# Kernel tuning notes

Hardware: AMD Instinct MI355X
Metric: run time of the kernel (lower is better)

## Reference

```python
import jax, jax.numpy as jnp
import numpy as np

PATCH = 12
IN_CH = 1
EMBED = 96
K_NEIGH = 5
N_NODES = 1024
B = 4
L_TIME = 2016  # 12 * 168 patches
CIN = IN_CH * (K_NEIGH + 1)


def setup_inputs() -> dict:
    key = jax.random.key(0)
    k1, k2, k3, k4 = jax.random.split(key, 4)
    long_term_history = jax.random.normal(k1, (B, N_NODES, IN_CH, L_TIME), dtype=jnp.float32)
    # positive adjacency weights (used as multinomial sampling probabilities)
    adj_mx = jax.random.uniform(k2, (N_NODES, N_NODES), dtype=jnp.float32, minval=1e-3, maxval=1.0)
    # Conv2d(in=CIN, out=EMBED, kernel=(PATCH,1)) -> weight [EMBED, CIN, PATCH]
    conv_w = jax.random.normal(k3, (EMBED, CIN, PATCH), dtype=jnp.float32) * 0.02
    conv_b = jax.random.normal(k4, (EMBED,), dtype=jnp.float32) * 0.02
    return {"long_term_history": long_term_history, "adj_mx": adj_mx,
            "conv_w": conv_w, "conv_b": conv_b}


def _sample_k_neighbors(adj_mx, k, key):
    # per-row multinomial with replacement via the Gumbel-max trick
    logits = jnp.log(adj_mx)                      # row-normalization is a constant shift
    g = jax.random.gumbel(key, (adj_mx.shape[0], k, adj_mx.shape[1]), dtype=adj_mx.dtype)
    return jnp.argmax(logits[:, None, :] + g, axis=-1)  # [N, k] int


def reference(long_term_history, adj_mx, conv_w, conv_b):
    b, n, c, lt = long_term_history.shape
    # adj_adjust_u = 1, adj_adjust_v = 0 (adjust_adj_mx=False) -> adjusted adj == adj
    sampled = _sample_k_neighbors(adj_mx, K_NEIGH, jax.random.key(42))  # [N, K]
    # batched neighbor gather: [B, N, K, C, L] -> [B, N, K*C, L]
    nb = long_term_history[:, sampled].reshape(b, n, K_NEIGH * c, lt)
    data = jnp.concatenate([long_term_history, nb], axis=2)  # [B, N, (K+1)*C, L]
    # patchify conv: kernel (PATCH,1), stride (PATCH,1) == per-patch GEMM
    p = lt // PATCH
    patches = data.reshape(b, n, CIN, p, PATCH)              # [B,N,Cin,P,patch]
    out = jnp.einsum('bncpt,oct->bnop', patches, conv_w) + conv_b[None, None, :, None]
    return out  # [B, N, EMBED, P]
```

## Files before the change

kernel.cpp:

```cpp
#include <hip/hip_runtime.h>
#include <cstdint>
#include <cstddef>

#define N_NODES 1024
#define K_NEIGH 5
#define L_TIME  2016
#define PATCHSZ 12
#define EMBED   96
#define CINX    6
#define P_CNT   168
#define KDOT    72
#define OUT_PER_BN (EMBED * P_CNT)

#define WS_WH 24576
#define WS_WL (24576 + 18432)

typedef __attribute__((ext_vector_type(8))) short   bf16x8;
typedef __attribute__((ext_vector_type(4))) float   f32x4;
typedef __attribute__((ext_vector_type(4))) unsigned int u32x4;

__device__ __forceinline__ uint32_t f2bf_bits(float f) {
  uint32_t u = __float_as_uint(f);
  return (u + 0x7fffu + ((u >> 16) & 1u)) >> 16;
}
__device__ __forceinline__ float bf_hi_f(uint32_t hb) { return __uint_as_float(hb << 16); }

__device__ __forceinline__ uint32_t rotl32(uint32_t x, int r) {
  return (x << r) | (x >> (32 - r));
}
__device__ __forceinline__ uint32_t threefry_bits(uint32_t hi, uint32_t lo) {
  const uint32_t ks0 = 0u, ks1 = 42u;
  const uint32_t ks2 = ks0 ^ ks1 ^ 0x1BD11BDAu;
  uint32_t x0 = hi + ks0, x1 = lo + ks1;
#define TF_ROUND(r) { x0 += x1; x1 = rotl32(x1, (r)); x1 ^= x0; }
  TF_ROUND(13) TF_ROUND(15) TF_ROUND(26) TF_ROUND(6)
  x0 += ks1; x1 += ks2 + 1u;
  TF_ROUND(17) TF_ROUND(29) TF_ROUND(16) TF_ROUND(24)
  x0 += ks2; x1 += ks0 + 2u;
  TF_ROUND(13) TF_ROUND(15) TF_ROUND(26) TF_ROUND(6)
  x0 += ks0; x1 += ks1 + 3u;
  TF_ROUND(17) TF_ROUND(29) TF_ROUND(16) TF_ROUND(24)
  x0 += ks1; x1 += ks2 + 4u;
  TF_ROUND(13) TF_ROUND(15) TF_ROUND(26) TF_ROUND(6)
  x0 += ks2; x1 += ks0 + 5u;
#undef TF_ROUND
  return x0 ^ x1;
}
__device__ __forceinline__ float gumbel_from_bits(uint32_t bits) {
  float f = __uint_as_float((bits >> 9) | 0x3f800000u) - 1.0f;
  f = fmaxf(f, 1.17549435e-38f);
  return -logf(-logf(f));
}

__global__ __launch_bounds__(256)
void wpack_kernel(const float* __restrict__ wgt, char* __restrict__ ws) {
  const int tid = threadIdx.x;
  for (int t = tid; t < 1152; t += 256) {
    const int L  = t & 63;
    const int mk = t >> 6;
    const int kc = mk % 3;
    const int m  = mk / 3;
    const int o  = m * 16 + (L & 15);
    const int kbase = kc * 32 + (L >> 4) * 8;
    uint32_t hb[8], lb[8];
    #pragma unroll
    for (int j = 0; j < 8; ++j) {
      const int k = kbase + j;
      float v = (k < KDOT) ? wgt[o * KDOT + k] : 0.0f;
      hb[j] = f2bf_bits(v);
      lb[j] = f2bf_bits(v - bf_hi_f(hb[j]));
    }
    u32x4 ph, pl;
    #pragma unroll
    for (int i = 0; i < 4; ++i) {
      ph[i] = hb[2*i] | (hb[2*i+1] << 16);
      pl[i] = lb[2*i] | (lb[2*i+1] << 16);
    }
    *reinterpret_cast<u32x4*>(ws + WS_WH + mk * 1024 + L * 16) = ph;
    *reinterpret_cast<u32x4*>(ws + WS_WL + mk * 1024 + L * 16) = pl;
  }
}

__global__ __launch_bounds__(1024)
void sample_kernel(const float* __restrict__ adj, int* __restrict__ sampled) {
  const int n = blockIdx.x;
  const int tid = threadIdx.x;
  const float la = logf(adj[(size_t)n * N_NODES + tid]);

  float best[K_NEIGH];
  int   bestj[K_NEIGH];
  #pragma unroll
  for (int k = 0; k < K_NEIGH; ++k) {
    uint32_t bits = threefry_bits(0u, (uint32_t)((n * K_NEIGH + k) * N_NODES + tid));
    best[k] = la + gumbel_from_bits(bits);
    bestj[k] = tid;
  }
  #pragma unroll
  for (int k = 0; k < K_NEIGH; ++k) {
    #pragma unroll
    for (int off = 32; off > 0; off >>= 1) {
      float ov = __shfl_down(best[k], off);
      int   oj = __shfl_down(bestj[k], off);
      if (ov > best[k] || (ov == best[k] && oj < bestj[k])) { best[k] = ov; bestj[k] = oj; }
    }
  }
  __shared__ float sv[16][K_NEIGH];
  __shared__ int   sj[16][K_NEIGH];
  if ((tid & 63) == 0) {
    #pragma unroll
    for (int k = 0; k < K_NEIGH; ++k) { sv[tid >> 6][k] = best[k]; sj[tid >> 6][k] = bestj[k]; }
  }
  __syncthreads();
  if (tid < K_NEIGH) {
    float b = sv[0][tid];
    int  bj = sj[0][tid];
    #pragma unroll
    for (int w = 1; w < 16; ++w) {
      if (sv[w][tid] > b || (sv[w][tid] == b && sj[w][tid] < bj)) { b = sv[w][tid]; bj = sj[w][tid]; }
    }
    sampled[n * K_NEIGH + tid] = bj;
  }
}

__global__ __launch_bounds__(256)
void embed_kernel(const float* __restrict__ hist, const char* __restrict__ ws,
                  const float* __restrict__ bias, const int* __restrict__ sampled,
                  float* __restrict__ out) {
  __shared__ __align__(16) char xlds[36864];
  char* XH = xlds;
  char* XL = xlds + 18432;

  const int tid  = threadIdx.x;
  const int L    = tid & 63;
  const int wave = tid >> 6;

  bf16x8 wh[18], wl[18];
  #pragma unroll
  for (int mk = 0; mk < 18; ++mk) {
    wh[mk] = __builtin_bit_cast(bf16x8, *reinterpret_cast<const u32x4*>(ws + WS_WH + mk*1024 + L*16));
    wl[mk] = __builtin_bit_cast(bf16x8, *reinterpret_cast<const u32x4*>(ws + WS_WL + mk*1024 + L*16));
  }
  float bv[6][4];
  #pragma unroll
  for (int m = 0; m < 6; ++m)
    #pragma unroll
    for (int i = 0; i < 4; ++i)
      bv[m][i] = bias[m * 16 + (L >> 4) * 4 + i];

  for (int bn = blockIdx.x; bn < 4 * N_NODES; bn += 512) {
    const int n = bn & (N_NODES - 1);
    const int b = bn >> 10;
    const float* rows[CINX];
    rows[0] = hist + (size_t)bn * L_TIME;
    #pragma unroll
    for (int k = 0; k < K_NEIGH; ++k)
      rows[k + 1] = hist + ((size_t)b * N_NODES + sampled[n * K_NEIGH + k]) * L_TIME;
    float* outbn = out + (size_t)bn * OUT_PER_BN;

    for (int h = 0; h < 2; ++h) {
      const int ncols  = h ? 80 : 96;
      const int ntasks = ncols * 12;
      for (int t = tid; t < ntasks; t += 256) {
        const int q   = t / ncols;
        const int ci  = t - q * ncols;
        const int p   = h * 96 + ci;
        const int ntl = ci >> 4;
        const int c16 = ci & 15;
        const int kc  = q >> 2;
        const int qg  = q & 3;
        char* dsth = XH + (ntl*3 + kc)*1024 + c16*64 + qg*16;
        char* dstl = XL + (ntl*3 + kc)*1024 + c16*64 + qg*16;
        u32x4 ph = {0,0,0,0}, pl = {0,0,0,0};
        if (q < 9 && p < P_CNT) {
          const int gk = q * 8;
          const int c0 = gk / 12,       t0 = gk - c0 * 12;
          const int c1 = (gk + 4) / 12, t1 = (gk + 4) - c1 * 12;
          const float4 f0 = *reinterpret_cast<const float4*>(rows[c0] + p * PATCHSZ + t0);
          const float4 f1 = *reinterpret_cast<const float4*>(rows[c1] + p * PATCHSZ + t1);
          const float v[8] = {f0.x, f0.y, f0.z, f0.w, f1.x, f1.y, f1.z, f1.w};
          uint32_t hb[8], lb[8];
          #pragma unroll
          for (int j = 0; j < 8; ++j) {
            hb[j] = f2bf_bits(v[j]);
            lb[j] = f2bf_bits(v[j] - bf_hi_f(hb[j]));
          }
          #pragma unroll
          for (int i = 0; i < 4; ++i) {
            ph[i] = hb[2*i] | (hb[2*i+1] << 16);
            pl[i] = lb[2*i] | (lb[2*i+1] << 16);
          }
        }
        *reinterpret_cast<u32x4*>(dsth) = ph;
        *reinterpret_cast<u32x4*>(dstl) = pl;
      }
      __syncthreads();
      const int T = h ? 5 : 6;
      for (int ntl = wave; ntl < T; ntl += 4) {
        f32x4 acc[6];
        #pragma unroll
        for (int m = 0; m < 6; ++m) acc[m] = {0.f, 0.f, 0.f, 0.f};
        #pragma unroll
        for (int kc = 0; kc < 3; ++kc) {
          const char* sh = XH + (ntl*3 + kc)*1024 + (L & 15)*64 + (L >> 4)*16;
          const char* sl = XL + (ntl*3 + kc)*1024 + (L & 15)*64 + (L >> 4)*16;
          const bf16x8 xh = __builtin_bit_cast(bf16x8, *reinterpret_cast<const u32x4*>(sh));
          const bf16x8 xl = __builtin_bit_cast(bf16x8, *reinterpret_cast<const u32x4*>(sl));
          #pragma unroll
          for (int m = 0; m < 6; ++m) {
            acc[m] = __builtin_amdgcn_mfma_f32_16x16x32_bf16(wh[m*3+kc], xh, acc[m], 0, 0, 0);
            acc[m] = __builtin_amdgcn_mfma_f32_16x16x32_bf16(wh[m*3+kc], xl, acc[m], 0, 0, 0);
            acc[m] = __builtin_amdgcn_mfma_f32_16x16x32_bf16(wl[m*3+kc], xh, acc[m], 0, 0, 0);
          }
        }
        const int p = h * 96 + ntl * 16 + (L & 15);
        if (p < P_CNT) {
          #pragma unroll
          for (int m = 0; m < 6; ++m) {
            const int o = m * 16 + (L >> 4) * 4;
            #pragma unroll
            for (int i = 0; i < 4; ++i)
              outbn[(size_t)(o + i) * P_CNT + p] = acc[m][i] + bv[m][i];
          }
        }
      }
      __syncthreads();
    }
  }
}

extern "C" void kernel_launch(void* const* d_in, const int* in_sizes, int n_in,
                              void* d_out, int out_size, void* d_ws, size_t ws_size,
                              hipStream_t stream) {
  const float* hist = (const float*)d_in[0];
  const float* adj  = (const float*)d_in[1];
  const float* wgt  = (const float*)d_in[2];
  const float* bias = (const float*)d_in[3];
  float* out = (float*)d_out;
  char* ws   = (char*)d_ws;
  int* sampled = (int*)d_ws;

  wpack_kernel<<<dim3(1), dim3(256), 0, stream>>>(wgt, ws);
  sample_kernel<<<dim3(N_NODES), dim3(1024), 0, stream>>>(adj, sampled);
  embed_kernel<<<dim3(512), dim3(256), 0, stream>>>(hist, ws, bias, sampled, out);
}
```

Measured before the change: 421.9 us.

## Load patch operands straight into MFMA registers, dropping LDS staging and barriers

Each wave now loads the input patch fragments it needs directly from global memory into registers, splits them into bf16 hi/lo, and feeds the MFMAs. This removes the shared-memory staging buffers and the two block barriers per half. The bias is folded into the accumulator's initial value, and output stores are nontemporal. The trade is a less coalesced global access pattern and no sharing of loaded data across waves, in exchange for higher occupancy and no synchronisation.

```diff
diff --git a/kernel.cpp b/kernel.cpp
--- a/kernel.cpp
+++ b/kernel.cpp
@@ -122,17 +122,28 @@
   }
 }
 
+__device__ __forceinline__ const float* sel_row(const float* r0, const float* r1,
+                                                const float* r2, const float* r3,
+                                                const float* r4, const float* r5,
+                                                int c) {
+  const float* p = r0;
+  p = (c == 1) ? r1 : p;
+  p = (c == 2) ? r2 : p;
+  p = (c == 3) ? r3 : p;
+  p = (c == 4) ? r4 : p;
+  p = (c == 5) ? r5 : p;
+  return p;
+}
+
 __global__ __launch_bounds__(256)
 void embed_kernel(const float* __restrict__ hist, const char* __restrict__ ws,
                   const float* __restrict__ bias, const int* __restrict__ sampled,
                   float* __restrict__ out) {
-  __shared__ __align__(16) char xlds[36864];
-  char* XH = xlds;
-  char* XL = xlds + 18432;
-
   const int tid  = threadIdx.x;
   const int L    = tid & 63;
   const int wave = tid >> 6;
+  const int g    = L >> 4;
+  const int col  = L & 15;
 
   bf16x8 wh[18], wl[18];
   #pragma unroll
@@ -140,43 +151,50 @@
     wh[mk] = __builtin_bit_cast(bf16x8, *reinterpret_cast<const u32x4*>(ws + WS_WH + mk*1024 + L*16));
     wl[mk] = __builtin_bit_cast(bf16x8, *reinterpret_cast<const u32x4*>(ws + WS_WL + mk*1024 + L*16));
   }
-  float bv[6][4];
+  f32x4 bv[6];
   #pragma unroll
   for (int m = 0; m < 6; ++m)
     #pragma unroll
     for (int i = 0; i < 4; ++i)
-      bv[m][i] = bias[m * 16 + (L >> 4) * 4 + i];
+      bv[m][i] = bias[m * 16 + g * 4 + i];
 
   for (int bn = blockIdx.x; bn < 4 * N_NODES; bn += 512) {
     const int n = bn & (N_NODES - 1);
     const int b = bn >> 10;
-    const float* rows[CINX];
-    rows[0] = hist + (size_t)bn * L_TIME;
-    #pragma unroll
-    for (int k = 0; k < K_NEIGH; ++k)
-      rows[k + 1] = hist + ((size_t)b * N_NODES + sampled[n * K_NEIGH + k]) * L_TIME;
+    const float* r0 = hist + (size_t)bn * L_TIME;
+    const float* r1 = hist + ((size_t)b * N_NODES + sampled[n * K_NEIGH + 0]) * L_TIME;
+    const float* r2 = hist + ((size_t)b * N_NODES + sampled[n * K_NEIGH + 1]) * L_TIME;
+    const float* r3 = hist + ((size_t)b * N_NODES + sampled[n * K_NEIGH + 2]) * L_TIME;
+    const float* r4 = hist + ((size_t)b * N_NODES + sampled[n * K_NEIGH + 3]) * L_TIME;
+    const float* r5 = hist + ((size_t)b * N_NODES + sampled[n * K_NEIGH + 4]) * L_TIME;
     float* outbn = out + (size_t)bn * OUT_PER_BN;
 
-    for (int h = 0; h < 2; ++h) {
-      const int ncols  = h ? 80 : 96;
-      const int ntasks = ncols * 12;
-      for (int t = tid; t < ntasks; t += 256) {
-        const int q   = t / ncols;
-        const int ci  = t - q * ncols;
-        const int p   = h * 96 + ci;
-        const int ntl = ci >> 4;
-        const int c16 = ci & 15;
-        const int kc  = q >> 2;
-        const int qg  = q & 3;
-        char* dsth = XH + (ntl*3 + kc)*1024 + c16*64 + qg*16;
-        char* dstl = XL + (ntl*3 + kc)*1024 + c16*64 + qg*16;
+    const float* a0[3];
+    const float* a1[3];
+    bool okk[3];
+    #pragma unroll
+    for (int kc = 0; kc < 3; ++kc) {
+      const int gk = kc * 32 + g * 8;
+      okk[kc] = (gk < KDOT);
+      const int c0 = gk / 12,       t0 = gk - c0 * 12;
+      const int c1 = (gk + 4) / 12, t1 = (gk + 4) - c1 * 12;
+      a0[kc] = sel_row(r0, r1, r2, r3, r4, r5, c0) + t0;
+      a1[kc] = sel_row(r0, r1, r2, r3, r4, r5, c1) + t1;
+    }
+
+    for (int ntl = wave; ntl < 11; ntl += 4) {
+      const int p = ntl * 16 + col;
+      const bool pok = (p < P_CNT);
+      f32x4 acc[6];
+      #pragma unroll
+      for (int m = 0; m < 6; ++m) acc[m] = bv[m];
+
+      #pragma unroll
+      for (int kc = 0; kc < 3; ++kc) {
         u32x4 ph = {0,0,0,0}, pl = {0,0,0,0};
-        if (q < 9 && p < P_CNT) {
-          const int gk = q * 8;
-          const int c0 = gk / 12,       t0 = gk - c0 * 12;
-          const int c1 = (gk + 4) / 12, t1 = (gk + 4) - c1 * 12;
-          const float4 f0 = *reinterpret_cast<const float4*>(rows[c0] + p * PATCHSZ + t0);
-          const float4 f1 = *reinterpret_cast<const float4*>(rows[c1] + p * PATCHSZ + t1);
+        if (okk[kc] && pok) {
+          const float4 f0 = *reinterpret_cast<const float4*>(a0[kc] + p * PATCHSZ);
+          const float4 f1 = *reinterpret_cast<const float4*>(a1[kc] + p * PATCHSZ);
           const float v[8] = {f0.x, f0.y, f0.z, f0.w, f1.x, f1.y, f1.z, f1.w};
           uint32_t hb[8], lb[8];
           #pragma unroll
@@ -190,40 +208,24 @@
             pl[i] = lb[2*i] | (lb[2*i+1] << 16);
           }
         }
-        *reinterpret_cast<u32x4*>(dsth) = ph;
-        *reinterpret_cast<u32x4*>(dstl) = pl;
-      }
-      __syncthreads();
-      const int T = h ? 5 : 6;
-      for (int ntl = wave; ntl < T; ntl += 4) {
-        f32x4 acc[6];
+        const bf16x8 xh = __builtin_bit_cast(bf16x8, ph);
+        const bf16x8 xl = __builtin_bit_cast(bf16x8, pl);
         #pragma unroll
-        for (int m = 0; m < 6; ++m) acc[m] = {0.f, 0.f, 0.f, 0.f};
-        #pragma unroll
-        for (int kc = 0; kc < 3; ++kc) {
-          const char* sh = XH + (ntl*3 + kc)*1024 + (L & 15)*64 + (L >> 4)*16;
-          const char* sl = XL + (ntl*3 + kc)*1024 + (L & 15)*64 + (L >> 4)*16;
-          const bf16x8 xh = __builtin_bit_cast(bf16x8, *reinterpret_cast<const u32x4*>(sh));
-          const bf16x8 xl = __builtin_bit_cast(bf16x8, *reinterpret_cast<const u32x4*>(sl));
-          #pragma unroll
-          for (int m = 0; m < 6; ++m) {
-            acc[m] = __builtin_amdgcn_mfma_f32_16x16x32_bf16(wh[m*3+kc], xh, acc[m], 0, 0, 0);
-            acc[m] = __builtin_amdgcn_mfma_f32_16x16x32_bf16(wh[m*3+kc], xl, acc[m], 0, 0, 0);
-            acc[m] = __builtin_amdgcn_mfma_f32_16x16x32_bf16(wl[m*3+kc], xh, acc[m], 0, 0, 0);
-          }
-        }
-        const int p = h * 96 + ntl * 16 + (L & 15);
-        if (p < P_CNT) {
-          #pragma unroll
-          for (int m = 0; m < 6; ++m) {
-            const int o = m * 16 + (L >> 4) * 4;
-            #pragma unroll
-            for (int i = 0; i < 4; ++i)
-              outbn[(size_t)(o + i) * P_CNT + p] = acc[m][i] + bv[m][i];
-          }
+        for (int m = 0; m < 6; ++m) {
+          acc[m] = __builtin_amdgcn_mfma_f32_16x16x32_bf16(wh[m*3+kc], xh, acc[m], 0, 0, 0);
+          acc[m] = __builtin_amdgcn_mfma_f32_16x16x32_bf16(wh[m*3+kc], xl, acc[m], 0, 0, 0);
+          acc[m] = __builtin_amdgcn_mfma_f32_16x16x32_bf16(wl[m*3+kc], xh, acc[m], 0, 0, 0);
         }
       }
-      __syncthreads();
+      if (pok) {
+        #pragma unroll
+        for (int m = 0; m < 6; ++m) {
+          const int o = m * 16 + g * 4;
+          #pragma unroll
+          for (int i = 0; i < 4; ++i)
+            __builtin_nontemporal_store(acc[m][i], &outbn[(size_t)(o + i) * P_CNT + p]);
+        }
+      }
     }
   }
 }
```

After: 461.7 us. +9.4%, slower.
